# Performance work log

Hardware: AMD Instinct MI355X
Metric: run time of the kernel (lower is better)

The kernel has to match this reference:

```python
import jax, jax.numpy as jnp
import numpy as np

B, S, D = 1, 2048, 2048
NH, NKV, HD = 32, 8, 64
EPS = 1e-5
SCALE = float(HD) ** 0.5


def _rope(x, cos, sin):
    # x: [b, h, s, hd]; cos/sin: [s, hd//2]; interleaved-pair rotary (executorch style)
    xr = x[..., 0::2]
    xi = x[..., 1::2]
    c = cos[None, None, :, :]
    s = sin[None, None, :, :]
    out_r = xr * c - xi * s
    out_i = xr * s + xi * c
    return jnp.stack([out_r, out_i], axis=-1).reshape(x.shape)


def _rmsnorm(x, w):
    var = jnp.mean(x * x, axis=-1, keepdims=True)
    return x * jax.lax.rsqrt(var + EPS) * w


def setup_inputs() -> dict:
    key = jax.random.key(0)
    ks = jax.random.split(key, 6)
    hidden_states = jax.random.normal(ks[0], (B, S, D), dtype=jnp.float32)
    # standard Llama rope tables, theta=10000
    inv_freq = 1.0 / (10000.0 ** (np.arange(0, HD, 2, dtype=np.float32) / HD))
    t = np.arange(S, dtype=np.float32)
    ang = np.outer(t, inv_freq)  # [S, HD//2]
    freqs_cos = jnp.asarray(np.cos(ang), dtype=jnp.float32)
    freqs_sin = jnp.asarray(np.sin(ang), dtype=jnp.float32)
    # additive causal mask [1,1,S,S]
    causal = jnp.tril(jnp.ones((S, S), dtype=bool))
    atten_mask = jnp.where(causal, 0.0, -1e9).astype(jnp.float32)[None, None]
    sd = 1.0 / np.sqrt(D)
    wq = jax.random.normal(ks[1], (NH * HD, D), dtype=jnp.float32) * sd
    wk = jax.random.normal(ks[2], (NKV * HD, D), dtype=jnp.float32) * sd
    wv = jax.random.normal(ks[3], (NKV * HD, D), dtype=jnp.float32) * sd
    wo = jax.random.normal(ks[4], (D, NH * HD), dtype=jnp.float32) * sd
    q_norm_w = jnp.ones((HD,), dtype=jnp.float32)
    k_norm_w = jnp.ones((HD,), dtype=jnp.float32)
    return dict(hidden_states=hidden_states, freqs_cos=freqs_cos, freqs_sin=freqs_sin,
                atten_mask=atten_mask, wq=wq, wk=wk, wv=wv, wo=wo,
                q_norm_w=q_norm_w, k_norm_w=k_norm_w)


def reference(hidden_states, freqs_cos, freqs_sin, atten_mask, wq, wk, wv, wo, q_norm_w, k_norm_w):
    b, s, _ = hidden_states.shape
    n_rep = NH // NKV
    # fused QKV projections (Linear: x @ W.T)
    q = (hidden_states @ wq.T).reshape(b, s, NH, HD).transpose(0, 2, 1, 3)   # [b,nh,s,hd]
    k = (hidden_states @ wk.T).reshape(b, s, NKV, HD).transpose(0, 2, 1, 3)  # [b,nkv,s,hd]
    v = (hidden_states @ wv.T).reshape(b, s, NKV, HD).transpose(0, 2, 1, 3)
    # RoPE, then QK RMSNorm (qk_norm_before_rope=False)
    q = _rope(q, freqs_cos, freqs_sin)
    k = _rope(k, freqs_cos, freqs_sin)
    q = _rmsnorm(q, q_norm_w)
    k = _rmsnorm(k, k_norm_w)
    # no KV cache (prefill): kh = k^T, vh = v, then GQA repeat
    kh = jnp.repeat(k, n_rep, axis=1)  # [b,nh,s,hd]
    vh = jnp.repeat(v, n_rep, axis=1)
    attn = jnp.einsum('bhqd,bhkd->bhqk', q, kh) / SCALE
    attn = jax.nn.softmax(attn + atten_mask, axis=-1)
    y = jnp.einsum('bhqk,bhkd->bhqd', attn, vh)
    y = y.transpose(0, 2, 1, 3).reshape(b, s, NH * HD)
    y = y @ wo.T
    # module returns (y, [kh], [vh]); kh stored transposed (b,nh,hd,s)
    return (y, kh.transpose(0, 1, 3, 2), vh)
```

## Files before the change

kernel.cpp:

```cpp
#include <hip/hip_runtime.h>
#include <cstdint>
#include <cstddef>

#define S_   2048
#define D_   2048
#define NH_  32
#define NKV_ 8
#define HD_  64

using bf16x8 = __attribute__((ext_vector_type(8))) __bf16;
using f32x4  = __attribute__((ext_vector_type(4))) float;

#define AS_GLOBAL(p) (const __attribute__((address_space(1))) void*)(p)
#define AS_LDS(p)    (__attribute__((address_space(3))) void*)(p)

__global__ __launch_bounds__(256) void cvt_all(
    const float* __restrict__ hs, const float* __restrict__ wq,
    const float* __restrict__ wk, const float* __restrict__ wv,
    const float* __restrict__ wo,
    __bf16* __restrict__ hs_bf, __bf16* __restrict__ wq_bf,
    __bf16* __restrict__ wk_bf, __bf16* __restrict__ wv_bf,
    __bf16* __restrict__ wo_bf) {
  int i = blockIdx.x * 256 + threadIdx.x;
  const float* src; __bf16* dst; int base;
  if (i < 1048576)      { src = hs; dst = hs_bf; base = 0; }
  else if (i < 2097152) { src = wq; dst = wq_bf; base = 1048576; }
  else if (i < 2359296) { src = wk; dst = wk_bf; base = 2097152; }
  else if (i < 2621440) { src = wv; dst = wv_bf; base = 2359296; }
  else                  { src = wo; dst = wo_bf; base = 2621440; }
  i -= base;
  const float4 v = reinterpret_cast<const float4*>(src)[i];
  __bf16 t[4] = {(__bf16)v.x, (__bf16)v.y, (__bf16)v.z, (__bf16)v.w};
  reinterpret_cast<uint2*>(dst)[i] = *reinterpret_cast<uint2*>(t);
}

__device__ __forceinline__ void gemm_tile_128(
    const __bf16* __restrict__ A, const __bf16* __restrict__ B,
    float* __restrict__ C, int K, int N, int m0, int n0) {
  __shared__ __align__(16) char lds[2][32768];
  const int tid = threadIdx.x;
  const int l = tid & 63;
  const int w = tid >> 6;
  const int l15 = l & 15, lg = l >> 4;
  const int wm = w >> 1, wn = w & 1;

  f32x4 acc[4][4] = {};

  const int srow   = tid >> 3;
  const int schunk = (tid & 7) ^ (srow & 7);
  const __bf16* gA = A + (size_t)(m0 + srow) * K + schunk * 8;
  const __bf16* gB = B + (size_t)(n0 + srow) * K + schunk * 8;
  const int ldst = tid * 16;
  const int nt = K >> 6;

#pragma unroll
  for (int i = 0; i < 4; ++i) {
    __builtin_amdgcn_global_load_lds(AS_GLOBAL(gA + (size_t)i*32*K),
                                     AS_LDS(&lds[0][i*4096 + ldst]), 16, 0, 0);
    __builtin_amdgcn_global_load_lds(AS_GLOBAL(gB + (size_t)i*32*K),
                                     AS_LDS(&lds[0][16384 + i*4096 + ldst]), 16, 0, 0);
  }
  __syncthreads();

  int cur = 0;
  for (int t = 0; t < nt; ++t) {
    if (t + 1 < nt) {
      const int k0 = (t + 1) * 64;
      char* dA = &lds[cur ^ 1][0];
      char* dB = &lds[cur ^ 1][16384];
#pragma unroll
      for (int i = 0; i < 4; ++i) {
        __builtin_amdgcn_global_load_lds(AS_GLOBAL(gA + (size_t)i*32*K + k0),
                                         AS_LDS(dA + i*4096 + ldst), 16, 0, 0);
        __builtin_amdgcn_global_load_lds(AS_GLOBAL(gB + (size_t)i*32*K + k0),
                                         AS_LDS(dB + i*4096 + ldst), 16, 0, 0);
      }
    }

    const char* ldsA = &lds[cur][0];
    const char* ldsB = &lds[cur][16384];
    bf16x8 af[4][2], bfr[4][2];
#pragma unroll
    for (int f = 0; f < 4; ++f) {
      const int arow = wm*64 + f*16 + l15;
      const int brow = wn*64 + f*16 + l15;
#pragma unroll
      for (int ks = 0; ks < 2; ++ks) {
        af[f][ks] = *reinterpret_cast<const bf16x8*>(
            ldsA + arow*128 + (((ks*4 + lg) ^ (arow & 7)) << 4));
        bfr[f][ks] = *reinterpret_cast<const bf16x8*>(
            ldsB + brow*128 + (((ks*4 + lg) ^ (brow & 7)) << 4));
      }
    }
#pragma unroll
    for (int mf = 0; mf < 4; ++mf)
#pragma unroll
      for (int nf = 0; nf < 4; ++nf) {
        acc[mf][nf] = __builtin_amdgcn_mfma_f32_16x16x32_bf16(
            af[mf][0], bfr[nf][0], acc[mf][nf], 0, 0, 0);
        acc[mf][nf] = __builtin_amdgcn_mfma_f32_16x16x32_bf16(
            af[mf][1], bfr[nf][1], acc[mf][nf], 0, 0, 0);
      }

    __syncthreads();
    cur ^= 1;
  }

#pragma unroll
  for (int mf = 0; mf < 4; ++mf)
#pragma unroll
    for (int nf = 0; nf < 4; ++nf)
#pragma unroll
      for (int r = 0; r < 4; ++r)
        C[(size_t)(m0 + wm*64 + mf*16 + lg*4 + r) * N + n0 + wn*64 + nf*16 + l15]
            = acc[mf][nf][r];
}

__global__ __launch_bounds__(256) void gemm_qkv(
    const __bf16* __restrict__ hs,
    const __bf16* __restrict__ wq, const __bf16* __restrict__ wk,
    const __bf16* __restrict__ wv,
    float* __restrict__ qp, float* __restrict__ kp, float* __restrict__ vp) {
  const int bx = blockIdx.x;
  const __bf16* Bm; float* Cm; int N, n0;
  if (bx < 16)      { Bm = wq; Cm = qp; N = 2048; n0 = bx * 128; }
  else if (bx < 20) { Bm = wk; Cm = kp; N = 512;  n0 = (bx - 16) * 128; }
  else              { Bm = wv; Cm = vp; N = 512;  n0 = (bx - 20) * 128; }
  gemm_tile_128(hs, Bm, Cm, 2048, N, blockIdx.y * 128, n0);
}

__global__ __launch_bounds__(256) void gemm_wo(
    const __bf16* __restrict__ ypre, const __bf16* __restrict__ wo,
    float* __restrict__ y) {
  gemm_tile_128(ypre, wo, y, 2048, 2048, blockIdx.y * 128, blockIdx.x * 128);
}

__global__ __launch_bounds__(256) void rope_norm_q(
    const float* __restrict__ q, const float* __restrict__ cosT,
    const float* __restrict__ sinT, const float* __restrict__ w,
    __bf16* __restrict__ qbf) {
  const int wid  = (int)((blockIdx.x * 256 + threadIdx.x) >> 6);
  const int lane = threadIdx.x & 63;
  const int s = wid >> 5;
  const int h = wid & 31;
  const size_t idx = (size_t)s*D_ + h*HD_ + lane;
  float val = q[idx];
  const float c  = cosT[s*32 + (lane >> 1)];
  const float sn = sinT[s*32 + (lane >> 1)];
  const float partner = __shfl_xor(val, 1);
  const float ro = (lane & 1) ? fmaf(partner, sn, val*c)
                              : fmaf(val, c, -partner*sn);
  float ssq = ro * ro;
#pragma unroll
  for (int off = 32; off >= 1; off >>= 1) ssq += __shfl_xor(ssq, off);
  const float rinv = rsqrtf(ssq * (1.0f/64.0f) + 1e-5f);
  qbf[idx] = (__bf16)(ro * rinv * w[lane] * 0.180336880111120426f);
}

__global__ __launch_bounds__(256) void rope_norm_k(
    float* __restrict__ k, const float* __restrict__ cosT,
    const float* __restrict__ sinT, const float* __restrict__ w,
    __bf16* __restrict__ kbf) {
  const int wid  = (int)((blockIdx.x * 256 + threadIdx.x) >> 6);
  const int lane = threadIdx.x & 63;
  const int s   = wid >> 3;
  const int kvh = wid & 7;
  const size_t idx = (size_t)s*(NKV_*HD_) + kvh*HD_ + lane;
  float val = k[idx];
  const float c  = cosT[s*32 + (lane >> 1)];
  const float sn = sinT[s*32 + (lane >> 1)];
  const float partner = __shfl_xor(val, 1);
  const float ro = (lane & 1) ? fmaf(partner, sn, val*c)
                              : fmaf(val, c, -partner*sn);
  float ssq = ro * ro;
#pragma unroll
  for (int off = 32; off >= 1; off >>= 1) ssq += __shfl_xor(ssq, off);
  const float rinv = rsqrtf(ssq * (1.0f/64.0f) + 1e-5f);
  const float res = ro * rinv * w[lane];
  k[idx] = res;
  kbf[idx] = (__bf16)res;
}

__global__ __launch_bounds__(256) void transpose_khT(
    const float* __restrict__ kpost, float* __restrict__ khT) {
  __shared__ float tl[64][68];
  const int s0  = blockIdx.x * 64;
  const int kvh = blockIdx.y;
  const int t = threadIdx.x;
  {
    const int d0 = (t & 15) * 4;
    const int sl = t >> 4;
#pragma unroll
    for (int rep = 0; rep < 4; ++rep) {
      const int srow = sl + rep*16;
      float4 v = *reinterpret_cast<const float4*>(
          &kpost[(size_t)(s0 + srow)*(NKV_*HD_) + kvh*HD_ + d0]);
      tl[d0+0][srow]=v.x; tl[d0+1][srow]=v.y; tl[d0+2][srow]=v.z; tl[d0+3][srow]=v.w;
    }
  }
  __syncthreads();
  {
    const int d  = t >> 2;
    const int s4 = (t & 3) * 16;
#pragma unroll
    for (int c = 0; c < 4; ++c) {
      float4 v;
      v.x = tl[d][s4+c*4+0]; v.y = tl[d][s4+c*4+1];
      v.z = tl[d][s4+c*4+2]; v.w = tl[d][s4+c*4+3];
#pragma unroll
      for (int r = 0; r < 4; ++r) {
        *reinterpret_cast<float4*>(
            &khT[((size_t)(kvh*4 + r)*HD_ + d)*S_ + s0 + s4 + c*4]) = v;
      }
    }
  }
}

__global__ __launch_bounds__(256) void transpose_v(
    const float* __restrict__ vp, float* __restrict__ vh,
    __bf16* __restrict__ vtbf) {
  __shared__ float tl[64][68];
  const int s0  = blockIdx.x * 64;
  const int kvh = blockIdx.y;
  const int t = threadIdx.x;
  const int srow = t >> 2, dc = (t & 3) * 16;
  const float* src = &vp[(size_t)(s0 + srow)*(NKV_*HD_) + kvh*HD_ + dc];
  float4 a = reinterpret_cast<const float4*>(src)[0];
  float4 b = reinterpret_cast<const float4*>(src)[1];
  float4 c = reinterpret_cast<const float4*>(src)[2];
  float4 d = reinterpret_cast<const float4*>(src)[3];
  *reinterpret_cast<float4*>(&tl[srow][dc])      = a;
  *reinterpret_cast<float4*>(&tl[srow][dc + 4])  = b;
  *reinterpret_cast<float4*>(&tl[srow][dc + 8])  = c;
  *reinterpret_cast<float4*>(&tl[srow][dc + 12]) = d;
#pragma unroll
  for (int r = 0; r < 4; ++r) {
    float* dst = &vh[((size_t)(kvh*4 + r)*S_ + s0 + srow)*HD_ + dc];
    reinterpret_cast<float4*>(dst)[0] = a;
    reinterpret_cast<float4*>(dst)[1] = b;
    reinterpret_cast<float4*>(dst)[2] = c;
    reinterpret_cast<float4*>(dst)[3] = d;
  }
  __syncthreads();
  const int dr = t >> 2, sc = (t & 3) * 16;
  __bf16 vals[16];
#pragma unroll
  for (int i = 0; i < 16; ++i) vals[i] = (__bf16)tl[sc + i][dr];
  uint4* dst = reinterpret_cast<uint4*>(&vtbf[((size_t)(kvh*64 + dr))*S_ + s0 + sc]);
  dst[0] = reinterpret_cast<uint4*>(vals)[0];
  dst[1] = reinterpret_cast<uint4*>(vals)[1];
}

__device__ __forceinline__ uint pack2bf(float a, float b) {
  __bf16 x = (__bf16)a, y = (__bf16)b;
  const uint ux = (uint)*reinterpret_cast<ushort*>(&x);
  const uint uy = (uint)*reinterpret_cast<ushort*>(&y);
  return ux | (uy << 16);
}

__device__ __forceinline__ void qk_tile_T(
    const char* kldh, bf16x8 qf0, bf16x8 qf1, f32x4 (&s_)[4],
    int l15, int lg) {
  __builtin_amdgcn_s_setprio(1);
#pragma unroll
  for (int nb = 0; nb < 4; ++nb) {
    const int row = nb*16 + l15;
    const int bc  = lg*16;
    const bf16x8 kb0 = *reinterpret_cast<const bf16x8*>(
        kldh + row*128 + ((bc)      ^ ((row & 7) << 4)));
    const bf16x8 kb1 = *reinterpret_cast<const bf16x8*>(
        kldh + row*128 + ((bc + 64) ^ ((row & 7) << 4)));
    f32x4 t = f32x4{0.f, 0.f, 0.f, 0.f};
    t = __builtin_amdgcn_mfma_f32_16x16x32_bf16(kb0, qf0, t, 0, 0, 0);
    t = __builtin_amdgcn_mfma_f32_16x16x32_bf16(kb1, qf1, t, 0, 0, 0);
    s_[nb] = t;
  }
  __builtin_amdgcn_s_setprio(0);
}

__device__ __forceinline__ void softmax_pv_T(
    f32x4 (&s_)[4], float& m_, float& l_, f32x4 (&o_)[4],
    char* pldw, const char* vbase, int l15, int lg) {
  float mx = fmaxf(fmaxf(s_[0][0], s_[0][1]), fmaxf(s_[0][2], s_[0][3]));
#pragma unroll
  for (int nb = 1; nb < 4; ++nb) {
    mx = fmaxf(mx, fmaxf(fmaxf(s_[nb][0], s_[nb][1]),
                         fmaxf(s_[nb][2], s_[nb][3])));
  }
  mx = fmaxf(mx, __shfl_xor(mx, 16));
  mx = fmaxf(mx, __shfl_xor(mx, 32));
  const float mnew = fmaxf(m_, mx);
  const float scl = exp2f(m_ - mnew);
  m_ = mnew;

  const int swz = (l15 & 7) << 4;
  float ls = 0.f;
#pragma unroll
  for (int nb = 0; nb < 4; ++nb) {
    float p0 = exp2f(s_[nb][0] - mnew);
    float p1 = exp2f(s_[nb][1] - mnew);
    float p2 = exp2f(s_[nb][2] - mnew);
    float p3 = exp2f(s_[nb][3] - mnew);
    ls += (p0 + p1) + (p2 + p3);
    *reinterpret_cast<uint*>(pldw + ((l15*128 + nb*32 + lg*8)     ^ swz)) = pack2bf(p0, p1);
    *reinterpret_cast<uint*>(pldw + ((l15*128 + nb*32 + lg*8 + 4) ^ swz)) = pack2bf(p2, p3);
  }
  ls += __shfl_xor(ls, 16);
  ls += __shfl_xor(ls, 32);
  l_ = l_*scl + ls;
#pragma unroll
  for (int nb = 0; nb < 4; ++nb) {
    o_[nb][0] *= scl; o_[nb][1] *= scl; o_[nb][2] *= scl; o_[nb][3] *= scl;
  }

  const bf16x8 pb0 = *reinterpret_cast<const bf16x8*>(
      pldw + ((l15*128 + lg*16)      ^ swz));
  const bf16x8 pb1 = *reinterpret_cast<const bf16x8*>(
      pldw + ((l15*128 + lg*16 + 64) ^ swz));

  __builtin_amdgcn_s_setprio(1);
#pragma unroll
  for (int nb = 0; nb < 4; ++nb) {
    const int row = nb*16 + l15;
    const int bc  = lg*16;
    const bf16x8 v0 = *reinterpret_cast<const bf16x8*>(
        vbase + row*128 + ((bc)      ^ ((row & 7) << 4)));
    const bf16x8 v1 = *reinterpret_cast<const bf16x8*>(
        vbase + row*128 + ((bc + 64) ^ ((row & 7) << 4)));
    f32x4 t = o_[nb];
    t = __builtin_amdgcn_mfma_f32_16x16x32_bf16(v0, pb0, t, 0, 0, 0);
    t = __builtin_amdgcn_mfma_f32_16x16x32_bf16(v1, pb1, t, 0, 0, 0);
    o_[nb] = t;
  }
  __builtin_amdgcn_s_setprio(0);
}

__device__ __forceinline__ void mask_diag_T(f32x4 (&s_)[4], int l15, int lg, int wg) {
  const int qrow = wg*16 + l15;
#pragma unroll
  for (int nb = 0; nb < 4; ++nb)
#pragma unroll
    for (int r = 0; r < 4; ++r)
      if (nb*16 + lg*4 + r > qrow) s_[nb][r] = -1e30f;
}

__global__ __launch_bounds__(512, 4) void flash_attn_mfma(
    const __bf16* __restrict__ qbf, const __bf16* __restrict__ kbf,
    const __bf16* __restrict__ vtbf, __bf16* __restrict__ ypre) {
  __shared__ __align__(16) char smem[49152];

  const int h   = blockIdx.y;
  const int pi  = blockIdx.x;
  const int qbA = pi, qbB = 31 - pi;
  const int SS  = (qbB >> 1) + 1;
  const int kvh = h >> 2;
  const int tid = threadIdx.x;
  const int l   = tid & 63;
  const int w   = tid >> 6;
  const int g   = tid >> 8;
  const int wg  = w & 3;
  const int l15 = l & 15;
  const int lg  = l >> 4;

  char* kldg = smem + g*8192;
  char* vtlg = smem + 16384 + g*8192;
  char* pldw = smem + 32768 + w*2048;

  const int ts = tid & 255;
  const int j  = ts >> 2;
  const int c0 = (ts & 3) * 16;
  const int b0 = (j*128 + c0*2)      ^ ((j & 7) << 4);
  const int b1 = (j*128 + c0*2 + 16) ^ ((j & 7) << 4);
  const __bf16* ksrc = kbf  + (size_t)(g*64 + j)*(NKV_*HD_) + kvh*HD_ + c0;
  const __bf16* vsrc = vtbf + (size_t)(kvh*64 + j)*S_ + g*64 + c0;

  bf16x8 qfA0, qfA1, qfB0, qfB1;
  {
    const __bf16* qa = qbf + (size_t)(qbA*64 + wg*16 + l15)*D_ + h*HD_ + lg*8;
    qfA0 = *reinterpret_cast<const bf16x8*>(qa);
    qfA1 = *reinterpret_cast<const bf16x8*>(qa + 32);
    const __bf16* qb = qbf + (size_t)(qbB*64 + wg*16 + l15)*D_ + h*HD_ + lg*8;
    qfB0 = *reinterpret_cast<const bf16x8*>(qb);
    qfB1 = *reinterpret_cast<const bf16x8*>(qb + 32);
  }

  f32x4 oA[4], oB[4];
#pragma unroll
  for (int nb = 0; nb < 4; ++nb) {
    oA[nb] = f32x4{0.f, 0.f, 0.f, 0.f};
    oB[nb] = f32x4{0.f, 0.f, 0.f, 0.f};
  }
  float mA = -1e30f, lA = 0.f, mB = -1e30f, lB = 0.f;

  uint4 kr0 = reinterpret_cast<const uint4*>(ksrc)[0];
  uint4 kr1 = reinterpret_cast<const uint4*>(ksrc + 8)[0];
  uint4 vr0 = reinterpret_cast<const uint4*>(vsrc)[0];
  uint4 vr1 = reinterpret_cast<const uint4*>(vsrc + 8)[0];

  for (int st = 0; st < SS; ++st) {
    __syncthreads();
    *reinterpret_cast<uint4*>(kldg + b0) = kr0;
    *reinterpret_cast<uint4*>(kldg + b1) = kr1;
    *reinterpret_cast<uint4*>(vtlg + b0) = vr0;
    *reinterpret_cast<uint4*>(vtlg + b1) = vr1;
    __syncthreads();

    if (st + 1 < SS) {
      const __bf16* kn = ksrc + (size_t)(st + 1)*128*(NKV_*HD_);
      const __bf16* vn = vsrc + (size_t)(st + 1)*128;
      kr0 = reinterpret_cast<const uint4*>(kn)[0];
      kr1 = reinterpret_cast<const uint4*>(kn + 8)[0];
      vr0 = reinterpret_cast<const uint4*>(vn)[0];
      vr1 = reinterpret_cast<const uint4*>(vn + 8)[0];
    }

    const int kt = 2*st + g;
    if (kt <= qbB) {
      f32x4 s_[4];
      qk_tile_T(kldg, qfB0, qfB1, s_, l15, lg);
      if (kt == qbB) mask_diag_T(s_, l15, lg, wg);
      softmax_pv_T(s_, mB, lB, oB, pldw, vtlg, l15, lg);
    }
    if (kt <= qbA) {
      f32x4 s_[4];
      qk_tile_T(kldg, qfA0, qfA1, s_, l15, lg);
      if (kt == qbA) mask_diag_T(s_, l15, lg, wg);
      softmax_pv_T(s_, mA, lA, oA, pldw, vtlg, l15, lg);
    }
  }

  float* ox = reinterpret_cast<float*>(smem);
  float* ml = reinterpret_cast<float*>(smem + 20480);
  float* po = ox + (wg*64 + l)*17;
  float* pm = ml + (wg*64 + l)*9;

  __syncthreads();
  if (g == 1) {
#pragma unroll
    for (int nb = 0; nb < 4; ++nb)
#pragma unroll
      for (int r = 0; r < 4; ++r) po[nb*4 + r] = oB[nb][r];
    pm[0] = mB; pm[1] = lB;
  }
  __syncthreads();
  if (g == 0) {
    const float m1 = pm[0], l1 = pm[1];
    const float m = fmaxf(mB, m1);
    const float s0 = exp2f(mB - m), s1 = exp2f(m1 - m);
    lB = lB*s0 + l1*s1;
#pragma unroll
    for (int nb = 0; nb < 4; ++nb)
#pragma unroll
      for (int r = 0; r < 4; ++r)
        oB[nb][r] = oB[nb][r]*s0 + po[nb*4 + r]*s1;
  }
  __syncthreads();
  if (g == 1) {
#pragma unroll
    for (int nb = 0; nb < 4; ++nb)
#pragma unroll
      for (int r = 0; r < 4; ++r) po[nb*4 + r] = oA[nb][r];
    pm[0] = mA; pm[1] = lA;
  }
  __syncthreads();
  if (g == 0) {
    const float m1 = pm[0], l1 = pm[1];
    const float m = fmaxf(mA, m1);
    const float s0 = exp2f(mA - m), s1 = exp2f(m1 - m);
    lA = lA*s0 + l1*s1;
#pragma unroll
    for (int nb = 0; nb < 4; ++nb)
#pragma unroll
      for (int r = 0; r < 4; ++r)
        oA[nb][r] = oA[nb][r]*s0 + po[nb*4 + r]*s1;

    const float rlA = 1.0f / lA, rlB = 1.0f / lB;
    const size_t rowA = (size_t)(qbA*64 + wg*16 + l15)*D_ + h*HD_;
    const size_t rowB = (size_t)(qbB*64 + wg*16 + l15)*D_ + h*HD_;
#pragma unroll
    for (int nb = 0; nb < 4; ++nb) {
      uint2 pa, pb;
      pa.x = pack2bf(oA[nb][0]*rlA, oA[nb][1]*rlA);
      pa.y = pack2bf(oA[nb][2]*rlA, oA[nb][3]*rlA);
      pb.x = pack2bf(oB[nb][0]*rlB, oB[nb][1]*rlB);
      pb.y = pack2bf(oB[nb][2]*rlB, oB[nb][3]*rlB);
      *reinterpret_cast<uint2*>(&ypre[rowA + nb*16 + lg*4]) = pa;
      *reinterpret_cast<uint2*>(&ypre[rowB + nb*16 + lg*4]) = pb;
    }
  }
}

extern "C" void kernel_launch(void* const* d_in, const int* in_sizes, int n_in,
                              void* d_out, int out_size, void* d_ws, size_t ws_size,
                              hipStream_t stream) {
  (void)in_sizes; (void)n_in; (void)out_size;
  const float* hs   = (const float*)d_in[0];
  const float* fcos = (const float*)d_in[1];
  const float* fsin = (const float*)d_in[2];
  const float* wq = (const float*)d_in[4];
  const float* wk = (const float*)d_in[5];
  const float* wv = (const float*)d_in[6];
  const float* wo = (const float*)d_in[7];
  const float* qw = (const float*)d_in[8];
  const float* kw = (const float*)d_in[9];

  float* out = (float*)d_out;
  float* y   = out;
  float* khT = out + 4194304;
  float* vh  = out + 8388608;

  __bf16* qbf   = (__bf16*)y;
  __bf16* kbf   = (__bf16*)((char*)y + 8*1024*1024);
  __bf16* vtbf  = (__bf16*)((char*)y + 10*1024*1024);
  __bf16* hs_bf = (__bf16*)khT;
  __bf16* wq_bf = (__bf16*)((char*)khT + 8*1024*1024);
  __bf16* wk_bf = (__bf16*)vh;
  __bf16* wv_bf = (__bf16*)((char*)vh + 2*1024*1024);

  const size_t need = (size_t)40 * 1024 * 1024;
  if (ws_size < need) return;
  char* ws = (char*)d_ws;
  float*  qp      = (float*)(ws);
  float*  kp      = (float*)(ws + 16*1024*1024);
  float*  vp      = (float*)(ws + 20*1024*1024);
  __bf16* ypre_bf = (__bf16*)(ws + 24*1024*1024);
  __bf16* wo_bf   = (__bf16*)(ws + 32*1024*1024);

  cvt_all<<<14336, 256, 0, stream>>>(hs, wq, wk, wv, wo,
                                     hs_bf, wq_bf, wk_bf, wv_bf, wo_bf);

  gemm_qkv<<<dim3(24, 16), 256, 0, stream>>>(hs_bf, wq_bf, wk_bf, wv_bf, qp, kp, vp);

  rope_norm_q<<<16384, 256, 0, stream>>>(qp, fcos, fsin, qw, qbf);
  rope_norm_k<<< 4096, 256, 0, stream>>>(kp, fcos, fsin, kw, kbf);

  transpose_khT<<<dim3(32, 8), 256, 0, stream>>>(kp, khT);
  transpose_v<<<dim3(32, 8), 256, 0, stream>>>(vp, vh, vtbf);

  flash_attn_mfma<<<dim3(16, 32), 512, 0, stream>>>(qbf, kbf, vtbf, ypre_bf);

  gemm_wo<<<dim3(16, 16), 256, 0, stream>>>(ypre_bf, wo_bf, y);
}
```

Before: 159.3 us.

## Use triple-buffered prefetch-depth-two pipeline for output projection GEMM

Adds a GEMM tile variant with three LDS stages that keeps two K-tiles of global-to-LDS loads in flight, using explicit vmcnt waits and a single barrier per iteration instead of a trailing syncthreads. Only the Wo projection kernel switches to it. The aim is to hide global memory latency better and cut one barrier per step. In exchange it uses 96KB of LDS per block, which can lower occupancy, and the hand-written waitcnt values have to match the number of outstanding loads exactly.

```diff
diff --git a/kernel.cpp b/kernel.cpp
--- a/kernel.cpp
+++ b/kernel.cpp
@@ -34,6 +34,33 @@
   reinterpret_cast<uint2*>(dst)[i] = *reinterpret_cast<uint2*>(t);
 }
 
+__device__ __forceinline__ void gemm_compute_step(
+    const char* ldsA, const char* ldsB, f32x4 (&acc)[4][4],
+    int l15, int lg, int wm, int wn) {
+  bf16x8 af[4][2], bfr[4][2];
+#pragma unroll
+  for (int f = 0; f < 4; ++f) {
+    const int arow = wm*64 + f*16 + l15;
+    const int brow = wn*64 + f*16 + l15;
+#pragma unroll
+    for (int ks = 0; ks < 2; ++ks) {
+      af[f][ks] = *reinterpret_cast<const bf16x8*>(
+          ldsA + arow*128 + (((ks*4 + lg) ^ (arow & 7)) << 4));
+      bfr[f][ks] = *reinterpret_cast<const bf16x8*>(
+          ldsB + brow*128 + (((ks*4 + lg) ^ (brow & 7)) << 4));
+    }
+  }
+#pragma unroll
+  for (int mf = 0; mf < 4; ++mf)
+#pragma unroll
+    for (int nf = 0; nf < 4; ++nf) {
+      acc[mf][nf] = __builtin_amdgcn_mfma_f32_16x16x32_bf16(
+          af[mf][0], bfr[nf][0], acc[mf][nf], 0, 0, 0);
+      acc[mf][nf] = __builtin_amdgcn_mfma_f32_16x16x32_bf16(
+          af[mf][1], bfr[nf][1], acc[mf][nf], 0, 0, 0);
+    }
+}
+
 __device__ __forceinline__ void gemm_tile_128(
     const __bf16* __restrict__ A, const __bf16* __restrict__ B,
     float* __restrict__ C, int K, int N, int m0, int n0) {
@@ -76,34 +103,78 @@
                                          AS_LDS(dB + i*4096 + ldst), 16, 0, 0);
       }
     }
-
-    const char* ldsA = &lds[cur][0];
-    const char* ldsB = &lds[cur][16384];
-    bf16x8 af[4][2], bfr[4][2];
-#pragma unroll
-    for (int f = 0; f < 4; ++f) {
-      const int arow = wm*64 + f*16 + l15;
-      const int brow = wn*64 + f*16 + l15;
-#pragma unroll
-      for (int ks = 0; ks < 2; ++ks) {
-        af[f][ks] = *reinterpret_cast<const bf16x8*>(
-            ldsA + arow*128 + (((ks*4 + lg) ^ (arow & 7)) << 4));
-        bfr[f][ks] = *reinterpret_cast<const bf16x8*>(
-            ldsB + brow*128 + (((ks*4 + lg) ^ (brow & 7)) << 4));
-      }
-    }
-#pragma unroll
-    for (int mf = 0; mf < 4; ++mf)
-#pragma unroll
-      for (int nf = 0; nf < 4; ++nf) {
-        acc[mf][nf] = __builtin_amdgcn_mfma_f32_16x16x32_bf16(
-            af[mf][0], bfr[nf][0], acc[mf][nf], 0, 0, 0);
-        acc[mf][nf] = __builtin_amdgcn_mfma_f32_16x16x32_bf16(
-            af[mf][1], bfr[nf][1], acc[mf][nf], 0, 0, 0);
-      }
-
+    gemm_compute_step(&lds[cur][0], &lds[cur][16384], acc, l15, lg, wm, wn);
     __syncthreads();
     cur ^= 1;
+  }
+
+#pragma unroll
+  for (int mf = 0; mf < 4; ++mf)
+#pragma unroll
+    for (int nf = 0; nf < 4; ++nf)
+#pragma unroll
+      for (int r = 0; r < 4; ++r)
+        C[(size_t)(m0 + wm*64 + mf*16 + lg*4 + r) * N + n0 + wn*64 + nf*16 + l15]
+            = acc[mf][nf][r];
+}
+
+__device__ __forceinline__ void gemm_tile_128_d2(
+    const __bf16* __restrict__ A, const __bf16* __restrict__ B,
+    float* __restrict__ C, int K, int N, int m0, int n0) {
+  __shared__ __align__(16) char lds[3][32768];
+  const int tid = threadIdx.x;
+  const int l = tid & 63;
+  const int w = tid >> 6;
+  const int l15 = l & 15, lg = l >> 4;
+  const int wm = w >> 1, wn = w & 1;
+
+  f32x4 acc[4][4] = {};
+
+  const int srow   = tid >> 3;
+  const int schunk = (tid & 7) ^ (srow & 7);
+  const __bf16* gA = A + (size_t)(m0 + srow) * K + schunk * 8;
+  const __bf16* gB = B + (size_t)(n0 + srow) * K + schunk * 8;
+  const int ldst = tid * 16;
+  const int nt = K >> 6;
+
+#pragma unroll
+  for (int i = 0; i < 4; ++i) {
+    __builtin_amdgcn_global_load_lds(AS_GLOBAL(gA + (size_t)i*32*K),
+                                     AS_LDS(&lds[0][i*4096 + ldst]), 16, 0, 0);
+    __builtin_amdgcn_global_load_lds(AS_GLOBAL(gB + (size_t)i*32*K),
+                                     AS_LDS(&lds[0][16384 + i*4096 + ldst]), 16, 0, 0);
+  }
+#pragma unroll
+  for (int i = 0; i < 4; ++i) {
+    __builtin_amdgcn_global_load_lds(AS_GLOBAL(gA + (size_t)i*32*K + 64),
+                                     AS_LDS(&lds[1][i*4096 + ldst]), 16, 0, 0);
+    __builtin_amdgcn_global_load_lds(AS_GLOBAL(gB + (size_t)i*32*K + 64),
+                                     AS_LDS(&lds[1][16384 + i*4096 + ldst]), 16, 0, 0);
+  }
+
+  char* p0 = &lds[0][0];
+  char* p1 = &lds[1][0];
+  char* p2 = &lds[2][0];
+
+  for (int t = 0; t < nt; ++t) {
+    if (t + 1 < nt) asm volatile("s_waitcnt vmcnt(8)" ::: "memory");
+    else            asm volatile("s_waitcnt vmcnt(0)" ::: "memory");
+    __builtin_amdgcn_s_barrier();
+
+    if (t + 2 < nt) {
+      const int k0 = (t + 2) * 64;
+#pragma unroll
+      for (int i = 0; i < 4; ++i) {
+        __builtin_amdgcn_global_load_lds(AS_GLOBAL(gA + (size_t)i*32*K + k0),
+                                         AS_LDS(p2 + i*4096 + ldst), 16, 0, 0);
+        __builtin_amdgcn_global_load_lds(AS_GLOBAL(gB + (size_t)i*32*K + k0),
+                                         AS_LDS(p2 + 16384 + i*4096 + ldst), 16, 0, 0);
+      }
+    }
+
+    gemm_compute_step(p0, p0 + 16384, acc, l15, lg, wm, wn);
+
+    char* tmp = p0; p0 = p1; p1 = p2; p2 = tmp;
   }
 
 #pragma unroll
@@ -132,7 +203,7 @@
 __global__ __launch_bounds__(256) void gemm_wo(
     const __bf16* __restrict__ ypre, const __bf16* __restrict__ wo,
     float* __restrict__ y) {
-  gemm_tile_128(ypre, wo, y, 2048, 2048, blockIdx.y * 128, blockIdx.x * 128);
+  gemm_tile_128_d2(ypre, wo, y, 2048, 2048, blockIdx.y * 128, blockIdx.x * 128);
 }
 
 __global__ __launch_bounds__(256) void rope_norm_q(
```

Result: faster. 154.2 us (-3.2%).
